# Kernel tuning notes

Measured on AMD Instinct MI355X. Metric: run time of the kernel, lower is better.

## Reference

```python
import jax, jax.numpy as jnp
import numpy as np

B, NT, NS, D, H = 4, 1024, 1024, 1024, 16
HD = D // H


def setup_inputs() -> dict:
    key = jax.random.key(0)
    ks = jax.random.split(key, 10)
    w_scale = (2.0 / (D + D)) ** 0.5  # xavier-ish
    return {
        "q": jax.random.normal(ks[0], (B, NT, D), jnp.float32),
        "k": jax.random.normal(ks[1], (B, NS, D), jnp.float32),
        "v": jax.random.normal(ks[2], (B, NS, D), jnp.float32),
        "q_w": jax.random.normal(ks[3], (D, D), jnp.float32) * w_scale,
        "k_w": jax.random.normal(ks[4], (D, D), jnp.float32) * w_scale,
        "v_w": jax.random.normal(ks[5], (D, D), jnp.float32) * w_scale,
        "out_w": jax.random.normal(ks[6], (D, D), jnp.float32) * w_scale,
        "b_q": jax.random.normal(ks[7], (1, D), jnp.float32) * 0.02,
        "b_k": jax.random.normal(ks[8], (1, D), jnp.float32) * 0.02,
        "b_v": jax.random.normal(ks[9], (1, D), jnp.float32) * 0.02,
        "b_out": jnp.zeros((1, D), jnp.float32),
        "attn_mask": jnp.zeros((NT, NS), jnp.float32),
    }


def reference(q, k, v, q_w, k_w, v_w, out_w, b_q, b_k, b_v, b_out, attn_mask):
    # Projections: torch f.linear(x, W, b) == x @ W.T + b
    qp = q @ q_w.T + b_q            # [B, Nt, D]
    kp = k @ k_w.T + b_k            # [B, Ns, D]
    vp = v @ v_w.T + b_v            # [B, Ns, D]
    # Split heads: D -> (H, HD)
    qh = qp.reshape(B, NT, H, HD)
    kh = kp.reshape(B, NS, H, HD)
    vh = vp.reshape(B, NS, H, HD)
    scale = 1.0 / jnp.sqrt(jnp.asarray(HD, qp.dtype))
    scores = jnp.einsum("bthd,bshd->bhts", qh * scale, kh)  # [B, H, Nt, Ns]
    scores = scores + attn_mask[None, None, :, :]
    attn_weights = jax.nn.softmax(scores, axis=-1)           # [B, H, Nt, Ns]
    ctx = jnp.einsum("bhts,bshd->bthd", attn_weights, vh)    # [B, Nt, H, HD]
    ctx = ctx.reshape(B, NT, D)
    attn_output = ctx @ out_w.T + b_out                      # [B, Nt, D]
    return attn_output, attn_weights
```

## Files before the change

kernel.cpp:

```cpp
#include <hip/hip_runtime.h>

#define B_  4
#define NT_ 1024
#define NS_ 1024
#define D_  1024
#define H_  16
#define HD_ 64

typedef unsigned short u16;
typedef __attribute__((ext_vector_type(8))) short short8;
typedef __attribute__((ext_vector_type(4))) float f32x4;
typedef __attribute__((ext_vector_type(4))) unsigned short u16x4;

static __device__ __forceinline__ u16 f2bf(float f) {
  unsigned u = __builtin_bit_cast(unsigned, f);
  u += 0x7fff + ((u >> 16) & 1);
  return (u16)(u >> 16);
}

static __device__ __forceinline__ float bf2f(u16 h) {
  return __builtin_bit_cast(float, (unsigned)h << 16);
}

static __device__ __forceinline__ f32x4 mfma16(short8 a, short8 b, f32x4 c) {
  return __builtin_amdgcn_mfma_f32_16x16x32_bf16(a, b, c, 0, 0, 0);
}

#define PIN(x) asm volatile("" : "+v"(x))

#define GLDS16(g, l) __builtin_amdgcn_global_load_lds( \
    (const __attribute__((address_space(1))) void*)(g), \
    (__attribute__((address_space(3))) void*)(l), 16, 0, 0)

struct CvtArgs {
  const float* src[4];
  u16* dst[4];
  int n[4];
};

__global__ __launch_bounds__(256) void cvt_kernel(CvtArgs a) {
  const int z = blockIdx.z;
  const float* __restrict__ src = a.src[z];
  u16* __restrict__ dst = a.dst[z];
  const int n = a.n[z];
  int i = (blockIdx.x * 256 + threadIdx.x) * 4;
  const int stride = gridDim.x * 256 * 4;
  for (; i < n; i += stride) {
    float4 v = *reinterpret_cast<const float4*>(src + i);
    u16x4 o;
    o[0] = f2bf(v.x); o[1] = f2bf(v.y); o[2] = f2bf(v.z); o[3] = f2bf(v.w);
    *reinterpret_cast<u16x4*>(dst + i) = o;
  }
}

template<int MODE, bool AF32>
static __device__ __forceinline__ void gemm_body(
    const void* __restrict__ Ain, const u16* __restrict__ Bt,
    const float* __restrict__ bias, void* __restrict__ Cout,
    const int N, const int K) {
  __shared__ u16 sA[128 * 32];
  __shared__ u16 sB[128 * 32];
  const int tid = threadIdx.x;
  const int wave = tid >> 6, lane = tid & 63;
  const int l15 = lane & 15, lq = lane >> 4;
  const size_t m0 = (size_t)blockIdx.y * 128;
  const size_t n0 = (size_t)blockIdx.x * 128;
  const int wr = (wave >> 1) * 64, wc = (wave & 1) * 64;
  f32x4 acc[4][4];
#pragma unroll
  for (int m = 0; m < 4; ++m)
#pragma unroll
    for (int n = 0; n < 4; ++n) acc[m][n] = (f32x4){0.f, 0.f, 0.f, 0.f};

  const int srow = lane >> 2;
  const int scol = (lane & 3) * 8;

  for (int kt = 0; kt < K; kt += 32) {
#pragma unroll
    for (int i = 0; i < 2; ++i) {
      const int q = wave * 2 + i;
      if (AF32) {
        const float* ga = (const float*)Ain + (m0 + q * 16 + srow) * K + kt + scol;
        float4 v0 = *reinterpret_cast<const float4*>(ga);
        float4 v1 = *reinterpret_cast<const float4*>(ga + 4);
        u16x4 p0, p1;
        p0[0] = f2bf(v0.x); p0[1] = f2bf(v0.y); p0[2] = f2bf(v0.z); p0[3] = f2bf(v0.w);
        p1[0] = f2bf(v1.x); p1[1] = f2bf(v1.y); p1[2] = f2bf(v1.z); p1[3] = f2bf(v1.w);
        u16* dst = sA + q * 512 + srow * 32 + scol;
        *reinterpret_cast<u16x4*>(dst) = p0;
        *reinterpret_cast<u16x4*>(dst + 4) = p1;
      } else {
        const u16* ga = (const u16*)Ain + (m0 + q * 16 + srow) * K + kt + scol;
        GLDS16(ga, sA + q * 512);
      }
      const u16* gb = Bt + (n0 + q * 16 + srow) * K + kt + scol;
      GLDS16(gb, sB + q * 512);
    }
    __syncthreads();
    short8 af[4], bfr[4];
#pragma unroll
    for (int m = 0; m < 4; ++m)
      af[m] = *reinterpret_cast<const short8*>(sA + (wr + m * 16 + l15) * 32 + lq * 8);
#pragma unroll
    for (int n = 0; n < 4; ++n)
      bfr[n] = *reinterpret_cast<const short8*>(sB + (wc + n * 16 + l15) * 32 + lq * 8);
#pragma unroll
    for (int m = 0; m < 4; ++m)
#pragma unroll
      for (int n = 0; n < 4; ++n)
        acc[m][n] = mfma16(af[m], bfr[n], acc[m][n]);
    __syncthreads();
  }
#pragma unroll
  for (int m = 0; m < 4; ++m) {
    const size_t row0 = m0 + wr + m * 16 + lq * 4;
#pragma unroll
    for (int n = 0; n < 4; ++n) {
      const size_t col = n0 + wc + n * 16 + l15;
      const float bv = bias[col];
      if (MODE == 2) {
        const int hh = (int)(col >> 6), hd = (int)(col & 63);
        const int bb = (int)(row0 >> 10), s0 = (int)(row0 & 1023);
        u16x4 o;
#pragma unroll
        for (int r = 0; r < 4; ++r) o[r] = f2bf(acc[m][n][r] + bv);
        *reinterpret_cast<u16x4*>(
            (u16*)Cout + (((size_t)(bb * H_ + hh) * HD_ + hd) << 10) + s0) = o;
      } else {
#pragma unroll
        for (int r = 0; r < 4; ++r) {
          const float v = acc[m][n][r] + bv;
          if (MODE == 1)
            ((u16*)Cout)[(row0 + r) * N + col] = f2bf(v);
          else
            ((float*)Cout)[(row0 + r) * N + col] = v;
        }
      }
    }
  }
}

__global__ __launch_bounds__(256) void qkv_gemm_kernel(
    const float* q, const float* k, const float* v,
    const u16* wq, const u16* wk, const u16* wv,
    const float* bq, const float* bk, const float* bv,
    u16* qp, u16* kp, u16* vpT) {
  const int z = blockIdx.z;
  if (z == 2) {
    gemm_body<2, true>(v, wv, bv, (void*)vpT, D_, D_);
  } else if (z == 1) {
    gemm_body<1, true>(k, wk, bk, (void*)kp, D_, D_);
  } else {
    gemm_body<1, true>(q, wq, bq, (void*)qp, D_, D_);
  }
}

__global__ __launch_bounds__(256) void oproj_kernel(
    const u16* __restrict__ A, const u16* __restrict__ Bt,
    const float* __restrict__ bias, float* __restrict__ C) {
  gemm_body<0, false>(A, Bt, bias, (void*)C, D_, D_);
}

__global__ __launch_bounds__(512, 2) void attn_kernel(
    const u16* __restrict__ qp, const u16* __restrict__ kp,
    const u16* __restrict__ vpT, const float* __restrict__ mask,
    float* __restrict__ wout, u16* __restrict__ ctx) {
  __shared__ u16 Pl[16 * 1024];
  __shared__ float ctxp[16 * 64];
  __shared__ float red[16 * 8];
  __shared__ float rfin[16];

  const int h = blockIdx.y, b = blockIdx.z;
  const int tid = threadIdx.x, wave = tid >> 6, lane = tid & 63;
  const int l15 = lane & 15, lq = lane >> 4;
  const int wcb = wave * 128;
  const int kh = wave >> 2, dq = wave & 3;

  const u16* kbase = kp + ((size_t)b * NS_) * D_ + h * HD_;
  short8 kf[8][2];
#pragma unroll
  for (int c = 0; c < 8; ++c)
#pragma unroll
    for (int ks = 0; ks < 2; ++ks)
      kf[c][ks] = *reinterpret_cast<const short8*>(
          kbase + (size_t)(wcb + c * 16 + l15) * D_ + ks * 32 + lq * 8);
#pragma unroll
  for (int c = 0; c < 8; ++c) { PIN(kf[c][0]); PIN(kf[c][1]); }

  short8 vf[16];
  const u16* vbase = vpT + ((size_t)((b * H_ + h) * HD_ + dq * 16 + l15)) * NS_
                   + kh * 512 + lq * 8;
#pragma unroll
  for (int ks = 0; ks < 16; ++ks)
    vf[ks] = *reinterpret_cast<const short8*>(vbase + ks * 32);
#pragma unroll
  for (int ks = 0; ks < 16; ++ks) PIN(vf[ks]);

  const u16* qbase = qp + ((size_t)(b * NT_ + blockIdx.x * 128)) * D_ + h * HD_;

  for (int it = 0; it < 8; ++it) {
    const int qt = blockIdx.x * 8 + it;

    short8 qf[2];
#pragma unroll
    for (int ks = 0; ks < 2; ++ks)
      qf[ks] = *reinterpret_cast<const short8*>(
          qbase + (size_t)(it * 16 + l15) * D_ + ks * 32 + lq * 8);

    f32x4 acc[8];
#pragma unroll
    for (int c = 0; c < 8; ++c) acc[c] = (f32x4){0.f, 0.f, 0.f, 0.f};
#pragma unroll
    for (int c = 0; c < 8; ++c)
#pragma unroll
      for (int ks = 0; ks < 2; ++ks)
        acc[c] = mfma16(kf[c][ks], qf[ks], acc[c]);

    const float* mbase = mask + (size_t)(qt * 16) * NS_ + wcb + lq * 4;
    {
      const int t = l15;
      u16* prow = Pl + t * 1024;
      const int swz = (t & 7) << 3;
      float s_part = 0.f;
#pragma unroll
      for (int c = 0; c < 8; ++c) {
        float4 mk = *reinterpret_cast<const float4*>(
            mbase + (size_t)l15 * NS_ + c * 16);
        float e0 = __expf(acc[c][0] * 0.125f + mk.x);
        float e1 = __expf(acc[c][1] * 0.125f + mk.y);
        float e2 = __expf(acc[c][2] * 0.125f + mk.z);
        float e3 = __expf(acc[c][3] * 0.125f + mk.w);
        s_part += (e0 + e1) + (e2 + e3);
        u16x4 p4;
        p4[0] = f2bf(e0); p4[1] = f2bf(e1); p4[2] = f2bf(e2); p4[3] = f2bf(e3);
        *reinterpret_cast<u16x4*>(prow + ((wcb + c * 16 + lq * 4) ^ swz)) = p4;
      }
      s_part += __shfl_xor(s_part, 16);
      s_part += __shfl_xor(s_part, 32);
      if (lane < 16) red[l15 * 8 + wave] = s_part;
    }

    __syncthreads();

    if (tid < 16) {
      float s = red[tid * 8];
#pragma unroll
      for (int w = 1; w < 8; ++w) s += red[tid * 8 + w];
      rfin[tid] = 1.0f / s;
    }

    {
      const int row = wave * 2 + (lane >> 5);
      float s = red[row * 8];
#pragma unroll
      for (int w = 1; w < 8; ++w) s += red[row * 8 + w];
      const float rinv = 1.0f / s;
      const int cb = (lane & 31) * 4;
      const u16* pr = Pl + row * 1024;
      const int sw = (row & 7) << 3;
      float* wrow = wout + ((size_t)((b * H_ + h) * NT_ + qt * 16 + row)) * NS_;
#pragma unroll
      for (int ch = 0; ch < 8; ++ch) {
        const int e = ch * 128 + cb;
        u16x4 p4 = *reinterpret_cast<const u16x4*>(pr + (e ^ sw));
        f32x4 w4;
        w4[0] = bf2f(p4[0]) * rinv; w4[1] = bf2f(p4[1]) * rinv;
        w4[2] = bf2f(p4[2]) * rinv; w4[3] = bf2f(p4[3]) * rinv;
        __builtin_nontemporal_store(w4, reinterpret_cast<f32x4*>(wrow + e));
      }
    }

    const u16* prow2 = Pl + l15 * 1024;
    const int swz2 = (l15 & 7) << 3;
    f32x4 acc2 = (f32x4){0.f, 0.f, 0.f, 0.f};
#pragma unroll
    for (int ks = 0; ks < 16; ++ks) {
      short8 pa = *reinterpret_cast<const short8*>(
          prow2 + ((kh * 512 + ks * 32 + lq * 8) ^ swz2));
      acc2 = mfma16(pa, vf[ks], acc2);
    }
    if (kh == 0) {
#pragma unroll
      for (int r = 0; r < 4; ++r)
        ctxp[(lq * 4 + r) * 64 + dq * 16 + l15] = acc2[r];
    }
    __syncthreads();

    if (kh == 1) {
      u16* cbase = ctx + ((size_t)(b * NT_ + qt * 16 + lq * 4)) * D_ + h * HD_ + dq * 16 + l15;
#pragma unroll
      for (int r = 0; r < 4; ++r) {
        const float v = (acc2[r] + ctxp[(lq * 4 + r) * 64 + dq * 16 + l15]) * rfin[lq * 4 + r];
        cbase[(size_t)r * D_] = f2bf(v);
      }
    }
  }
}

extern "C" void kernel_launch(void* const* d_in, const int* in_sizes, int n_in,
                              void* d_out, int out_size, void* d_ws, size_t ws_size,
                              hipStream_t stream) {
  const float* q   = (const float*)d_in[0];
  const float* k   = (const float*)d_in[1];
  const float* v   = (const float*)d_in[2];
  const float* q_w = (const float*)d_in[3];
  const float* k_w = (const float*)d_in[4];
  const float* v_w = (const float*)d_in[5];
  const float* o_w = (const float*)d_in[6];
  const float* b_q = (const float*)d_in[7];
  const float* b_k = (const float*)d_in[8];
  const float* b_v = (const float*)d_in[9];
  const float* b_o = (const float*)d_in[10];
  const float* msk = (const float*)d_in[11];

  float* out = (float*)d_out;
  float* wout = out + (size_t)B_ * NT_ * D_;

  u16* wq  = (u16*)d_ws;
  u16* wk  = wq + 1048576;
  u16* wv  = wk + 1048576;
  u16* wo  = wv + 1048576;
  u16* qp  = wo + 1048576;
  u16* kp  = qp + 4194304;
  u16* vpT = kp + 4194304;
  u16* ctx = vpT + 4194304;

  CvtArgs ca;
  ca.src[0] = q_w; ca.dst[0] = wq; ca.n[0] = D_ * D_;
  ca.src[1] = k_w; ca.dst[1] = wk; ca.n[1] = D_ * D_;
  ca.src[2] = v_w; ca.dst[2] = wv; ca.n[2] = D_ * D_;
  ca.src[3] = o_w; ca.dst[3] = wo; ca.n[3] = D_ * D_;
  cvt_kernel<<<dim3(256, 1, 4), 256, 0, stream>>>(ca);

  qkv_gemm_kernel<<<dim3(8, 32, 3), 256, 0, stream>>>(
      q, k, v, wq, wk, wv, b_q, b_k, b_v, qp, kp, vpT);

  attn_kernel<<<dim3(8, 16, 4), 512, 0, stream>>>(qp, kp, vpT, msk, wout, ctx);

  oproj_kernel<<<dim3(8, 32), 256, 0, stream>>>(ctx, wo, b_o, out);
}
```

Measured before the change: 188.7 us.

## Prefetch next Q tile and bf16 mask, double-buffer P to reorder attention loop

The additive mask is converted to bf16 in the existing conversion kernel, which halves the mask bytes the attention kernel reads. The next iteration's Q fragments and mask values are prefetched into registers during the current one. The P buffer and reduction scratch are double-buffered so the PV matmul and ctx write can run before the normalized weight store, letting that store overlap the next iteration. This adds LDS use (a second 32KB P buffer), which may reduce occupancy, and rounds the mask to bf16, losing precision for non-zero masks.

```diff
diff --git a/kernel.cpp b/kernel.cpp
--- a/kernel.cpp
+++ b/kernel.cpp
@@ -33,9 +33,9 @@
     (__attribute__((address_space(3))) void*)(l), 16, 0, 0)
 
 struct CvtArgs {
-  const float* src[4];
-  u16* dst[4];
-  int n[4];
+  const float* src[5];
+  u16* dst[5];
+  int n[5];
 };
 
 __global__ __launch_bounds__(256) void cvt_kernel(CvtArgs a) {
@@ -163,11 +163,11 @@
 
 __global__ __launch_bounds__(512, 2) void attn_kernel(
     const u16* __restrict__ qp, const u16* __restrict__ kp,
-    const u16* __restrict__ vpT, const float* __restrict__ mask,
+    const u16* __restrict__ vpT, const u16* __restrict__ mbf,
     float* __restrict__ wout, u16* __restrict__ ctx) {
-  __shared__ u16 Pl[16 * 1024];
+  __shared__ u16 Pl[2][16 * 1024];
   __shared__ float ctxp[16 * 64];
-  __shared__ float red[16 * 8];
+  __shared__ float red[2][16 * 8];
   __shared__ float rfin[16];
 
   const int h = blockIdx.y, b = blockIdx.z;
@@ -197,15 +197,23 @@
   for (int ks = 0; ks < 16; ++ks) PIN(vf[ks]);
 
   const u16* qbase = qp + ((size_t)(b * NT_ + blockIdx.x * 128)) * D_ + h * HD_;
+  const u16* mbb = mbf + wcb + lq * 4;
+
+  short8 qf[2];
+  u16x4 mk[8];
+  {
+    const u16* qrow = qbase + (size_t)l15 * D_;
+    qf[0] = *reinterpret_cast<const short8*>(qrow + lq * 8);
+    qf[1] = *reinterpret_cast<const short8*>(qrow + 32 + lq * 8);
+    const u16* mrow = mbb + (size_t)(blockIdx.x * 128 + l15) * NS_;
+#pragma unroll
+    for (int c = 0; c < 8; ++c)
+      mk[c] = *reinterpret_cast<const u16x4*>(mrow + c * 16);
+  }
 
   for (int it = 0; it < 8; ++it) {
+    const int p = it & 1;
     const int qt = blockIdx.x * 8 + it;
-
-    short8 qf[2];
-#pragma unroll
-    for (int ks = 0; ks < 2; ++ks)
-      qf[ks] = *reinterpret_cast<const short8*>(
-          qbase + (size_t)(it * 16 + l15) * D_ + ks * 32 + lq * 8);
 
     f32x4 acc[8];
 #pragma unroll
@@ -216,20 +224,17 @@
       for (int ks = 0; ks < 2; ++ks)
         acc[c] = mfma16(kf[c][ks], qf[ks], acc[c]);
 
-    const float* mbase = mask + (size_t)(qt * 16) * NS_ + wcb + lq * 4;
     {
       const int t = l15;
-      u16* prow = Pl + t * 1024;
+      u16* prow = Pl[p] + t * 1024;
       const int swz = (t & 7) << 3;
       float s_part = 0.f;
 #pragma unroll
       for (int c = 0; c < 8; ++c) {
-        float4 mk = *reinterpret_cast<const float4*>(
-            mbase + (size_t)l15 * NS_ + c * 16);
-        float e0 = __expf(acc[c][0] * 0.125f + mk.x);
-        float e1 = __expf(acc[c][1] * 0.125f + mk.y);
-        float e2 = __expf(acc[c][2] * 0.125f + mk.z);
-        float e3 = __expf(acc[c][3] * 0.125f + mk.w);
+        float e0 = __expf(acc[c][0] * 0.125f + bf2f(mk[c][0]));
+        float e1 = __expf(acc[c][1] * 0.125f + bf2f(mk[c][1]));
+        float e2 = __expf(acc[c][2] * 0.125f + bf2f(mk[c][2]));
+        float e3 = __expf(acc[c][3] * 0.125f + bf2f(mk[c][3]));
         s_part += (e0 + e1) + (e2 + e3);
         u16x4 p4;
         p4[0] = f2bf(e0); p4[1] = f2bf(e1); p4[2] = f2bf(e2); p4[3] = f2bf(e3);
@@ -237,26 +242,61 @@
       }
       s_part += __shfl_xor(s_part, 16);
       s_part += __shfl_xor(s_part, 32);
-      if (lane < 16) red[l15 * 8 + wave] = s_part;
+      if (lane < 16) red[p][l15 * 8 + wave] = s_part;
     }
 
     __syncthreads();
 
     if (tid < 16) {
-      float s = red[tid * 8];
-#pragma unroll
-      for (int w = 1; w < 8; ++w) s += red[tid * 8 + w];
+      float s = red[p][tid * 8];
+#pragma unroll
+      for (int w = 1; w < 8; ++w) s += red[p][tid * 8 + w];
       rfin[tid] = 1.0f / s;
+    }
+
+    const u16* prow2 = Pl[p] + l15 * 1024;
+    const int swz2 = (l15 & 7) << 3;
+    f32x4 acc2 = (f32x4){0.f, 0.f, 0.f, 0.f};
+#pragma unroll
+    for (int ks = 0; ks < 16; ++ks) {
+      short8 pa = *reinterpret_cast<const short8*>(
+          prow2 + ((kh * 512 + ks * 32 + lq * 8) ^ swz2));
+      acc2 = mfma16(pa, vf[ks], acc2);
+    }
+    if (kh == 0) {
+#pragma unroll
+      for (int r = 0; r < 4; ++r)
+        ctxp[(lq * 4 + r) * 64 + dq * 16 + l15] = acc2[r];
+    }
+    __syncthreads();
+
+    if (kh == 1) {
+      u16* cbase = ctx + ((size_t)(b * NT_ + qt * 16 + lq * 4)) * D_ + h * HD_ + dq * 16 + l15;
+#pragma unroll
+      for (int r = 0; r < 4; ++r) {
+        const float v = (acc2[r] + ctxp[(lq * 4 + r) * 64 + dq * 16 + l15]) * rfin[lq * 4 + r];
+        cbase[(size_t)r * D_] = f2bf(v);
+      }
+    }
+
+    if (it < 7) {
+      const u16* qrow = qbase + (size_t)((it + 1) * 16 + l15) * D_;
+      qf[0] = *reinterpret_cast<const short8*>(qrow + lq * 8);
+      qf[1] = *reinterpret_cast<const short8*>(qrow + 32 + lq * 8);
+      const u16* mrow = mbb + (size_t)((blockIdx.x * 8 + it + 1) * 16 + l15) * NS_;
+#pragma unroll
+      for (int c = 0; c < 8; ++c)
+        mk[c] = *reinterpret_cast<const u16x4*>(mrow + c * 16);
     }
 
     {
       const int row = wave * 2 + (lane >> 5);
-      float s = red[row * 8];
-#pragma unroll
-      for (int w = 1; w < 8; ++w) s += red[row * 8 + w];
+      float s = red[p][row * 8];
+#pragma unroll
+      for (int w = 1; w < 8; ++w) s += red[p][row * 8 + w];
       const float rinv = 1.0f / s;
       const int cb = (lane & 31) * 4;
-      const u16* pr = Pl + row * 1024;
+      const u16* pr = Pl[p] + row * 1024;
       const int sw = (row & 7) << 3;
       float* wrow = wout + ((size_t)((b * H_ + h) * NT_ + qt * 16 + row)) * NS_;
 #pragma unroll
@@ -267,31 +307,6 @@
         w4[0] = bf2f(p4[0]) * rinv; w4[1] = bf2f(p4[1]) * rinv;
         w4[2] = bf2f(p4[2]) * rinv; w4[3] = bf2f(p4[3]) * rinv;
         __builtin_nontemporal_store(w4, reinterpret_cast<f32x4*>(wrow + e));
-      }
-    }
-
-    const u16* prow2 = Pl + l15 * 1024;
-    const int swz2 = (l15 & 7) << 3;
-    f32x4 acc2 = (f32x4){0.f, 0.f, 0.f, 0.f};
-#pragma unroll
-    for (int ks = 0; ks < 16; ++ks) {
-      short8 pa = *reinterpret_cast<const short8*>(
-          prow2 + ((kh * 512 + ks * 32 + lq * 8) ^ swz2));
-      acc2 = mfma16(pa, vf[ks], acc2);
-    }
-    if (kh == 0) {
-#pragma unroll
-      for (int r = 0; r < 4; ++r)
-        ctxp[(lq * 4 + r) * 64 + dq * 16 + l15] = acc2[r];
-    }
-    __syncthreads();
-
-    if (kh == 1) {
-      u16* cbase = ctx + ((size_t)(b * NT_ + qt * 16 + lq * 4)) * D_ + h * HD_ + dq * 16 + l15;
-#pragma unroll
-      for (int r = 0; r < 4; ++r) {
-        const float v = (acc2[r] + ctxp[(lq * 4 + r) * 64 + dq * 16 + l15]) * rfin[lq * 4 + r];
-        cbase[(size_t)r * D_] = f2bf(v);
       }
     }
   }
@@ -324,18 +339,20 @@
   u16* kp  = qp + 4194304;
   u16* vpT = kp + 4194304;
   u16* ctx = vpT + 4194304;
+  u16* mbf = ctx + 4194304;
 
   CvtArgs ca;
-  ca.src[0] = q_w; ca.dst[0] = wq; ca.n[0] = D_ * D_;
-  ca.src[1] = k_w; ca.dst[1] = wk; ca.n[1] = D_ * D_;
-  ca.src[2] = v_w; ca.dst[2] = wv; ca.n[2] = D_ * D_;
-  ca.src[3] = o_w; ca.dst[3] = wo; ca.n[3] = D_ * D_;
-  cvt_kernel<<<dim3(256, 1, 4), 256, 0, stream>>>(ca);
+  ca.src[0] = q_w; ca.dst[0] = wq;  ca.n[0] = D_ * D_;
+  ca.src[1] = k_w; ca.dst[1] = wk;  ca.n[1] = D_ * D_;
+  ca.src[2] = v_w; ca.dst[2] = wv;  ca.n[2] = D_ * D_;
+  ca.src[3] = o_w; ca.dst[3] = wo;  ca.n[3] = D_ * D_;
+  ca.src[4] = msk; ca.dst[4] = mbf; ca.n[4] = NT_ * NS_;
+  cvt_kernel<<<dim3(256, 1, 5), 256, 0, stream>>>(ca);
 
   qkv_gemm_kernel<<<dim3(8, 32, 3), 256, 0, stream>>>(
       q, k, v, wq, wk, wv, b_q, b_k, b_v, qp, kp, vpT);
 
-  attn_kernel<<<dim3(8, 16, 4), 512, 0, stream>>>(qp, kp, vpT, msk, wout, ctx);
+  attn_kernel<<<dim3(8, 16, 4), 512, 0, stream>>>(qp, kp, vpT, mbf, wout, ctx);
 
   oproj_kernel<<<dim3(8, 32), 256, 0, stream>>>(ctx, wo, b_o, out);
 }
```

Result: slower. 202.1 us (+7.1%).
